# Kernel tuning notes

Measured on AMD Instinct MI355X. Metric: run time of the kernel, lower is better.

Reference implementation:

```python
import jax, jax.numpy as jnp
import numpy as np
from jax import lax

IMG_W = 800.0
CONF_THRESHOLD = 0.5
MAX_MATCHES = 8
N_PROPOSALS = 65536
N_TARGETS = 128


def setup_inputs() -> dict:
    key = jax.random.key(0)
    ks = jax.random.split(key, 14)
    N, T = N_PROPOSALS, N_TARGETS
    # raw (pre-normalization) geometric scores: theta in [0, 360) deg,
    # start-point / distance errors in [0, 2*img_w) px (exercises the clamp branch)
    theta = jax.random.uniform(ks[0], (N, T), jnp.float32) * 360.0
    xys = jax.random.uniform(ks[1], (N, T), jnp.float32) * (2.0 * IMG_W)
    dist = jax.random.uniform(ks[2], (N, T), jnp.float32) * (2.0 * IMG_W)
    pos = jax.random.uniform(ks[3], (N, T), jnp.float32)
    neg = jax.random.uniform(ks[4], (N, T), jnp.float32)
    iou = jax.random.uniform(ks[5], (N, T), jnp.float32)
    targets = jax.random.uniform(ks[6], (T, 4), jnp.float32)
    # MatchNet: small MLP 6 -> 64 -> 32 -> 1 with ReLU hidden, sigmoid output
    W1 = jax.random.normal(ks[7], (6, 64), jnp.float32) * 0.3
    b1 = jnp.zeros((64,), jnp.float32)
    W2 = jax.random.normal(ks[8], (64, 32), jnp.float32) * 0.3
    b2 = jnp.zeros((32,), jnp.float32)
    W3 = jax.random.normal(ks[9], (32, 1), jnp.float32) * 0.3
    b3 = jnp.zeros((1,), jnp.float32)
    return {
        "theta_score_deep": theta, "start_xys_score_deep": xys,
        "distances_score_deep": dist, "pos_score_deep": pos,
        "neg_score_deep": neg, "iou_deep": iou, "targets": targets,
        "W1": W1, "b1": b1, "W2": W2, "b2": b2, "W3": W3, "b3": b3,
    }


def _norm(x, cap):
    # torch: x[x > cap] = cap; x = 1 - x / cap
    return 1.0 - jnp.minimum(x, cap) / cap


def _matchnet(feats, W1, b1, W2, b2, W3, b3):
    # feats: [N, T, 6] -> scores [N, T]
    h = jax.nn.relu(feats @ W1 + b1)
    h = jax.nn.relu(h @ W2 + b2)
    return jax.nn.sigmoid(h @ W3 + b3)[..., 0]


def reference(theta_score_deep, start_xys_score_deep, distances_score_deep,
              pos_score_deep, neg_score_deep, iou_deep, targets,
              W1, b1, W2, b2, W3, b3):
    theta = _norm(theta_score_deep, 180.0)
    xys = _norm(start_xys_score_deep, IMG_W)
    dist = _norm(distances_score_deep, IMG_W)
    feats = jnp.stack([theta, xys, dist, pos_score_deep, neg_score_deep, iou_deep],
                      axis=-1)                      # [N, T, 6]
    scores = _matchnet(feats, W1, b1, W2, b2, W3, b3)  # [N, T]
    scores = jnp.where(scores < CONF_THRESHOLD, 0.0, scores)
    # top-k proposals per target, fully batched over the target dim
    vals, idx = lax.top_k(scores.T, MAX_MATCHES)    # [T, K] each
    # the torch loop visits targets in descending order of targets[:, 1]
    order = jnp.argsort(-targets[:, 1], stable=True)  # [T]
    rows = idx[order].reshape(-1).astype(jnp.int32)   # [T*K]
    cols = jnp.repeat(order.astype(jnp.int32), MAX_MATCHES)  # [T*K]
    valid = (vals[order] > 0.0).reshape(-1)           # [T*K] bool
    # fixed-shape padded equivalent of the original's variable-length cat:
    # (rows[valid], cols[valid]) reproduces the torch output exactly
    return rows, cols, valid
```

## Files before the change

### kernel.cpp

```cpp
#include <hip/hip_runtime.h>


typedef unsigned int   u32;
typedef unsigned short u16;
typedef short s8v  __attribute__((ext_vector_type(8)));
typedef float f4v  __attribute__((ext_vector_type(4)));

#define N_PROP   65536
#define N_TGT    128
#define N_PAIR   (N_PROP * N_TGT)
#define CAP      4096
#define MARGIN   0.15f
#define NCHUNK   512

static __device__ __forceinline__ u32 packbf(float a, float b) {
  return __builtin_amdgcn_perm(__float_as_uint(b), __float_as_uint(a), 0x07060302u);
}
static __device__ __forceinline__ float bf16_rne(float x) {
  u32 u = __float_as_uint(x);
  u = u + 0x7fffu + ((u >> 16) & 1u);
  return __uint_as_float(u & 0xffff0000u);
}
static __device__ __forceinline__ float bf2f(u16 u) {
  return __uint_as_float(((u32)u) << 16);
}
static __device__ __forceinline__ s8v mk_frag(u32 a, u32 b, u32 c, u32 d) {
  union { u32 u[4]; s8v v; } x;
  x.u[0] = a; x.u[1] = b; x.u[2] = c; x.u[3] = d;
  return x.v;
}
static __device__ __forceinline__ f4v MF16(s8v a, s8v b, f4v c) {
  return __builtin_amdgcn_mfma_f32_16x16x32_bf16(a, b, c, 0, 0, 0);
}

__global__ __launch_bounds__(256) void k1_mfma(
    const float* __restrict__ p_th, const float* __restrict__ p_xy,
    const float* __restrict__ p_di, const float* __restrict__ p_po,
    const float* __restrict__ p_ne, const float* __restrict__ p_io,
    const float* __restrict__ W1, const float* __restrict__ b1,
    const float* __restrict__ W2, const float* __restrict__ b2,
    const float* __restrict__ W3, const float* __restrict__ b3,
    u16* __restrict__ lgout)
{
  const int tid = threadIdx.x;
  const int l   = tid & 63;
  const int lo4 = l & 15;
  const int q   = (l >> 4) & 3;

  s8v aw1[4];
#pragma unroll
  for (int mt = 0; mt < 4; ++mt) {
    float v[8];
#pragma unroll
    for (int j = 0; j < 8; ++j) {
      const int k = 8 * q + j;
      float x = 0.0f;
      if (k < 6)       x = W1[k * 64 + 16 * mt + lo4];
      else if (k == 6) x = b1[16 * mt + lo4];
      v[j] = bf16_rne(x);
    }
    aw1[mt] = mk_frag(packbf(v[0], v[1]), packbf(v[2], v[3]),
                      packbf(v[4], v[5]), packbf(v[6], v[7]));
  }

  s8v aw2[2][2];
#pragma unroll
  for (int mt = 0; mt < 2; ++mt)
#pragma unroll
    for (int c = 0; c < 2; ++c) {
      float v[8];
#pragma unroll
      for (int j = 0; j < 8; ++j)
        v[j] = bf16_rne(W2[(32 * c + 8 * q + j) * 32 + 16 * mt + lo4]);
      aw2[mt][c] = mk_frag(packbf(v[0], v[1]), packbf(v[2], v[3]),
                           packbf(v[4], v[5]), packbf(v[6], v[7]));
    }

  float b2l[2][4], w3l[2][4];
#pragma unroll
  for (int mt = 0; mt < 2; ++mt)
#pragma unroll
    for (int r = 0; r < 4; ++r) {
      const int row = 16 * mt + 4 * q + r;
      b2l[mt][r] = b2[row];
      w3l[mt][r] = W3[row];
    }
  const float b3s = b3[0];
  const f4v Z4 = {};

  const bool q0  = (q == 0);
  const bool qlo = (q < 2);
  const int srcA = ((q & 1) << 5) + lo4;
  const int srcB = srcA + 16;

  const int nwaves = (gridDim.x * blockDim.x) >> 6;
  const int w0 = (blockIdx.x * blockDim.x + tid) >> 6;
  const int NGRP = N_PAIR / 16;

#pragma unroll 2
  for (int g = w0; g < NGRP; g += nwaves) {
    const int idx = g * 16 + lo4;
    const float x0 = p_th[idx], x1 = p_xy[idx], x2 = p_di[idx];
    const float x3 = p_po[idx], x4 = p_ne[idx], x5 = p_io[idx];
    const float f0 = fmaf(fminf(x0, 180.0f), -(1.0f / 180.0f), 1.0f);
    const float f1 = fmaf(fminf(x1, 800.0f), -(1.0f / 800.0f), 1.0f);
    const float f2 = fmaf(fminf(x2, 800.0f), -(1.0f / 800.0f), 1.0f);

    const s8v bfeat = mk_frag(q0 ? packbf(f0, f1) : 0u,
                              q0 ? packbf(f2, x3) : 0u,
                              q0 ? packbf(x4, x5) : 0u,
                              q0 ? 0x00003f80u : 0u);

    u32 hl[4], hh[4];
#pragma unroll
    for (int mt = 0; mt < 4; ++mt) {
      const f4v hv = MF16(aw1[mt], bfeat, Z4);
      hl[mt] = packbf(fmaxf(hv[0], 0.0f), fmaxf(hv[1], 0.0f));
      hh[mt] = packbf(fmaxf(hv[2], 0.0f), fmaxf(hv[3], 0.0f));
    }

    s8v b2f[2];
#pragma unroll
    for (int c = 0; c < 2; ++c) {
      const int mlo = 2 * c, mhi = 2 * c + 1;
      const u32 a0 = (u32)__shfl((int)hl[mlo], srcA, 64);
      const u32 a1 = (u32)__shfl((int)hh[mlo], srcA, 64);
      const u32 a2 = (u32)__shfl((int)hl[mlo], srcB, 64);
      const u32 a3 = (u32)__shfl((int)hh[mlo], srcB, 64);
      const u32 g0 = (u32)__shfl((int)hl[mhi], srcA, 64);
      const u32 g1 = (u32)__shfl((int)hh[mhi], srcA, 64);
      const u32 g2 = (u32)__shfl((int)hl[mhi], srcB, 64);
      const u32 g3 = (u32)__shfl((int)hh[mhi], srcB, 64);
      b2f[c] = mk_frag(qlo ? a0 : g0, qlo ? a1 : g1,
                       qlo ? a2 : g2, qlo ? a3 : g3);
    }

    f4v acc0 = Z4, acc1 = Z4;
    acc0 = MF16(aw2[0][0], b2f[0], acc0);
    acc0 = MF16(aw2[0][1], b2f[1], acc0);
    acc1 = MF16(aw2[1][0], b2f[0], acc1);
    acc1 = MF16(aw2[1][1], b2f[1], acc1);

    float part = 0.0f;
#pragma unroll
    for (int r = 0; r < 4; ++r) {
      part = fmaf(w3l[0][r], fmaxf(acc0[r] + b2l[0][r], 0.0f), part);
      part = fmaf(w3l[1][r], fmaxf(acc1[r] + b2l[1][r], 0.0f), part);
    }
    part += __shfl_xor(part, 16, 64);
    part += __shfl_xor(part, 32, 64);

    if (q0)
      lgout[idx] = (u16)(__float_as_uint(part + b3s) >> 16);
  }
}

__global__ void k2a_part(const u16* __restrict__ lg, float* __restrict__ pval)
{
  const int t = threadIdx.x;
  const int c = blockIdx.x;
  const size_t base = (size_t)c * 128 * 128 + t;
  float v[8];
#pragma unroll
  for (int q = 0; q < 8; ++q) v[q] = -3.4e38f;
#pragma unroll 4
  for (int i = 0; i < 128; ++i) {
    const float x = bf2f(lg[base + (size_t)i * 128]);
    if (x > v[7]) {
      int k = 7;
      while (k > 0 && x > v[k - 1]) { v[k] = v[k - 1]; --k; }
      v[k] = x;
    }
  }
  float* o = pval + ((size_t)c * 128 + t) * 8;
#pragma unroll
  for (int q = 0; q < 8; ++q) o[q] = v[q];
}

__global__ void k2b_merge(const float* __restrict__ pval, float* __restrict__ tau)
{
  __shared__ float sm[64 * 8];
  const int t = blockIdx.x;
  const int i = threadIdx.x;
  float v[8];
#pragma unroll
  for (int q = 0; q < 8; ++q) v[q] = -3.4e38f;
  for (int e = i; e < NCHUNK * 8; e += 64) {
    const float x = pval[(size_t)(e >> 3) * 1024 + (size_t)t * 8 + (e & 7)];
    if (x > v[7]) {
      int k = 7;
      while (k > 0 && x > v[k - 1]) { v[k] = v[k - 1]; --k; }
      v[k] = x;
    }
  }
#pragma unroll
  for (int q = 0; q < 8; ++q) sm[i * 8 + q] = v[q];
  __syncthreads();
  if (i == 0) {
    float w[8];
#pragma unroll
    for (int q = 0; q < 8; ++q) w[q] = -3.4e38f;
    for (int e = 0; e < 512; ++e) {
      const float x = sm[e];
      if (x > w[7]) {
        int k = 7;
        while (k > 0 && x > w[k - 1]) { w[k] = w[k - 1]; --k; }
        w[k] = x;
      }
    }
    tau[t] = w[7] - MARGIN;
  }
}

__global__ void k2c_cand(const u16* __restrict__ lg, const float* __restrict__ tau,
                         int* __restrict__ cnt, int* __restrict__ cand)
{
  const int t = threadIdx.x;
  const int c = blockIdx.x;
  const int n0 = c * 128;
  const float ta = tau[t];
#pragma unroll 4
  for (int i = 0; i < 128; ++i) {
    const int n = n0 + i;
    const float x = bf2f(lg[(size_t)n * 128 + t]);
    if (x >= ta || n < 16) {
      const int p = atomicAdd(&cnt[t], 1);
      if (p < CAP) cand[(size_t)t * CAP + p] = n;
    }
  }
}

__global__ __launch_bounds__(256) void k3_refine(
    const float* __restrict__ p_th, const float* __restrict__ p_xy,
    const float* __restrict__ p_di, const float* __restrict__ p_po,
    const float* __restrict__ p_ne, const float* __restrict__ p_io,
    const float* __restrict__ W1, const float* __restrict__ b1,
    const float* __restrict__ W2, const float* __restrict__ b2,
    const float* __restrict__ W3, const float* __restrict__ b3,
    const int* __restrict__ cnt, const int* __restrict__ cand,
    int* __restrict__ t8i, float* __restrict__ t8k)
{
  __shared__ float wl[2561];
  __shared__ float ck[CAP];
  __shared__ int   cnid[CAP];
  const int t = blockIdx.x;
  const int tid = threadIdx.x;

  for (int i = tid; i < 2561; i += 256) {
    float x;
    if (i < 384)       x = W1[i];
    else if (i < 448)  x = b1[i - 384];
    else if (i < 2496) x = W2[i - 448];
    else if (i < 2528) x = b2[i - 2496];
    else if (i < 2560) x = W3[i - 2528];
    else               x = b3[0];
    wl[i] = x;
  }
  __syncthreads();
  const float* W1L = wl;
  const float* b1L = wl + 384;
  const float* W2L = wl + 448;
  const float* b2L = wl + 2496;
  const float* W3L = wl + 2528;
  const float  b3s = wl[2560];

  int m = cnt[t];
  if (m > CAP) m = CAP;

  for (int i = tid; i < m; i += 256) {
    const int n = cand[(size_t)t * CAP + i];
    const size_t off = (size_t)n * 128 + t;
    float f[6];
    f[0] = 1.0f - fminf(p_th[off], 180.0f) / 180.0f;
    f[1] = 1.0f - fminf(p_xy[off], 800.0f) / 800.0f;
    f[2] = 1.0f - fminf(p_di[off], 800.0f) / 800.0f;
    f[3] = p_po[off]; f[4] = p_ne[off]; f[5] = p_io[off];

    float h1[64];
#pragma unroll
    for (int j = 0; j < 64; ++j) {
      float s = b1L[j];
#pragma unroll
      for (int k = 0; k < 6; ++k) s = fmaf(f[k], W1L[k * 64 + j], s);
      h1[j] = fmaxf(s, 0.0f);
    }
    float h2[32];
#pragma unroll
    for (int j = 0; j < 32; ++j) {
      float s = b2L[j];
#pragma unroll
      for (int k = 0; k < 64; ++k) s = fmaf(h1[k], W2L[k * 32 + j], s);
      h2[j] = fmaxf(s, 0.0f);
    }
    float lo = b3s;
#pragma unroll
    for (int k = 0; k < 32; ++k) lo = fmaf(h2[k], W3L[k], lo);
    const float sg = 1.0f / (1.0f + expf(-lo));
    ck[i]   = (sg < 0.5f) ? 0.0f : sg;
    cnid[i] = n;
  }
  __syncthreads();

  if (tid == 0) {
    float bv[8]; int bi[8];
#pragma unroll
    for (int q = 0; q < 8; ++q) { bv[q] = -1.0f; bi[q] = 0x7fffffff; }
    for (int i = 0; i < m; ++i) {
      const float x = ck[i];
      const int   n = cnid[i];
      if (x > bv[7] || (x == bv[7] && n < bi[7])) {
        int k = 7;
        while (k > 0 && (x > bv[k - 1] || (x == bv[k - 1] && n < bi[k - 1]))) {
          bv[k] = bv[k - 1]; bi[k] = bi[k - 1]; --k;
        }
        bv[k] = x; bi[k] = n;
      }
    }
#pragma unroll
    for (int q = 0; q < 8; ++q) {
      t8i[t * 8 + q] = bi[q];
      t8k[t * 8 + q] = bv[q];
    }
  }
}

__global__ void k4_final(const float* __restrict__ targets,
                         const int* __restrict__ t8i, const float* __restrict__ t8k,
                         int* __restrict__ out)
{
  __shared__ float key[128];
  __shared__ int   ord[128];
  const int i = threadIdx.x;
  key[i] = targets[i * 4 + 1];
  __syncthreads();
  const float ki = key[i];
  int r = 0;
  for (int j = 0; j < 128; ++j) {
    const float kj = key[j];
    r += (kj > ki) || (kj == ki && j < i);
  }
  ord[r] = i;
  __syncthreads();
  const int src = ord[i];
#pragma unroll
  for (int k = 0; k < 8; ++k) {
    out[i * 8 + k]        = t8i[src * 8 + k];
    out[1024 + i * 8 + k] = src;
    out[2048 + i * 8 + k] = (t8k[src * 8 + k] > 0.0f) ? 1 : 0;
  }
}

extern "C" void kernel_launch(void* const* d_in, const int* in_sizes, int n_in,
                              void* d_out, int out_size, void* d_ws, size_t ws_size,
                              hipStream_t stream)
{
  const float* p_th = (const float*)d_in[0];
  const float* p_xy = (const float*)d_in[1];
  const float* p_di = (const float*)d_in[2];
  const float* p_po = (const float*)d_in[3];
  const float* p_ne = (const float*)d_in[4];
  const float* p_io = (const float*)d_in[5];
  const float* tgt  = (const float*)d_in[6];
  const float* W1   = (const float*)d_in[7];
  const float* b1   = (const float*)d_in[8];
  const float* W2   = (const float*)d_in[9];
  const float* b2   = (const float*)d_in[10];
  const float* W3   = (const float*)d_in[11];
  const float* b3   = (const float*)d_in[12];

  char* base = (char*)d_ws;
  u16*   lg   = (u16*)  (base);
  float* pval = (float*)(base + 16777216);
  int*   cand = (int*)  (base + 16777216);
  float* tau  = (float*)(base + 18874368);
  int*   cnt  = (int*)  (base + 18874880);
  int*   t8i  = (int*)  (base + 18875392);
  float* t8k  = (float*)(base + 18879488);

  hipMemsetAsync(cnt, 0, 128 * sizeof(int), stream);

  k1_mfma<<<2048, 256, 0, stream>>>(p_th, p_xy, p_di, p_po, p_ne, p_io,
                                    W1, b1, W2, b2, W3, b3, lg);
  k2a_part<<<NCHUNK, 128, 0, stream>>>(lg, pval);
  k2b_merge<<<128, 64, 0, stream>>>(pval, tau);
  k2c_cand<<<NCHUNK, 128, 0, stream>>>(lg, tau, cnt, cand);
  k3_refine<<<128, 256, 0, stream>>>(p_th, p_xy, p_di, p_po, p_ne, p_io,
                                     W1, b1, W2, b2, W3, b3,
                                     cnt, cand, t8i, t8k);
  k4_final<<<1, 128, 0, stream>>>(tgt, t8i, t8k, (int*)d_out);
}
```

Before: 691.8 us.

## Permute W2 fragment layout to feed layer-1 MFMA output directly, dropping shuffles

```diff
diff --git a/kernel.cpp b/kernel.cpp
--- a/kernel.cpp
+++ b/kernel.cpp
@@ -33,7 +33,7 @@
   return __builtin_amdgcn_mfma_f32_16x16x32_bf16(a, b, c, 0, 0, 0);
 }
 
-__global__ __launch_bounds__(256) void k1_mfma(
+__global__ __launch_bounds__(256, 4) void k1_mfma(
     const float* __restrict__ p_th, const float* __restrict__ p_xy,
     const float* __restrict__ p_di, const float* __restrict__ p_po,
     const float* __restrict__ p_ne, const float* __restrict__ p_io,
@@ -70,8 +70,10 @@
     for (int c = 0; c < 2; ++c) {
       float v[8];
 #pragma unroll
-      for (int j = 0; j < 8; ++j)
-        v[j] = bf16_rne(W2[(32 * c + 8 * q + j) * 32 + 16 * mt + lo4]);
+      for (int j = 0; j < 8; ++j) {
+        const int u = 16 * (2 * c + (j >> 2)) + 4 * q + (j & 3);
+        v[j] = bf16_rne(W2[u * 32 + 16 * mt + lo4]);
+      }
       aw2[mt][c] = mk_frag(packbf(v[0], v[1]), packbf(v[2], v[3]),
                            packbf(v[4], v[5]), packbf(v[6], v[7]));
     }
@@ -88,10 +90,7 @@
   const float b3s = b3[0];
   const f4v Z4 = {};
 
-  const bool q0  = (q == 0);
-  const bool qlo = (q < 2);
-  const int srcA = ((q & 1) << 5) + lo4;
-  const int srcB = srcA + 16;
+  const bool q0 = (q == 0);
 
   const int nwaves = (gridDim.x * blockDim.x) >> 6;
   const int w0 = (blockIdx.x * blockDim.x + tid) >> 6;
@@ -119,27 +118,14 @@
       hh[mt] = packbf(fmaxf(hv[2], 0.0f), fmaxf(hv[3], 0.0f));
     }
 
-    s8v b2f[2];
-#pragma unroll
-    for (int c = 0; c < 2; ++c) {
-      const int mlo = 2 * c, mhi = 2 * c + 1;
-      const u32 a0 = (u32)__shfl((int)hl[mlo], srcA, 64);
-      const u32 a1 = (u32)__shfl((int)hh[mlo], srcA, 64);
-      const u32 a2 = (u32)__shfl((int)hl[mlo], srcB, 64);
-      const u32 a3 = (u32)__shfl((int)hh[mlo], srcB, 64);
-      const u32 g0 = (u32)__shfl((int)hl[mhi], srcA, 64);
-      const u32 g1 = (u32)__shfl((int)hh[mhi], srcA, 64);
-      const u32 g2 = (u32)__shfl((int)hl[mhi], srcB, 64);
-      const u32 g3 = (u32)__shfl((int)hh[mhi], srcB, 64);
-      b2f[c] = mk_frag(qlo ? a0 : g0, qlo ? a1 : g1,
-                       qlo ? a2 : g2, qlo ? a3 : g3);
-    }
+    const s8v b2f0 = mk_frag(hl[0], hh[0], hl[1], hh[1]);
+    const s8v b2f1 = mk_frag(hl[2], hh[2], hl[3], hh[3]);
 
     f4v acc0 = Z4, acc1 = Z4;
-    acc0 = MF16(aw2[0][0], b2f[0], acc0);
-    acc0 = MF16(aw2[0][1], b2f[1], acc0);
-    acc1 = MF16(aw2[1][0], b2f[0], acc1);
-    acc1 = MF16(aw2[1][1], b2f[1], acc1);
+    acc0 = MF16(aw2[0][0], b2f0, acc0);
+    acc0 = MF16(aw2[0][1], b2f1, acc0);
+    acc1 = MF16(aw2[1][0], b2f0, acc1);
+    acc1 = MF16(aw2[1][1], b2f1, acc1);
 
     float part = 0.0f;
 #pragma unroll
```

Measured after the change: 665.6 us. 1.04x faster.
